# Performance work log

Hardware: AMD Instinct MI355X
Metric: run time of the kernel (lower is better)

## Reference

```python
import jax, jax.numpy as jnp
import numpy as np

NUM_HEADS = 12

def setup_inputs() -> dict:
    key = jax.random.key(0)
    ks = jax.random.split(key, 6)
    B, N, C, P = 16, 785, 768, 48
    return {
        "x": jax.random.normal(ks[0], (B, N, C), jnp.float32),
        "qkv_w": jax.random.normal(ks[1], (3 * C, C), jnp.float32) * 0.02,
        "pos_emb": jax.random.normal(ks[2], (N, N, P), jnp.float32) * 0.02,
        "pos_proj_w": jax.random.normal(ks[3], (NUM_HEADS, P), jnp.float32) * 0.02,
        "proj_w": jax.random.normal(ks[4], (C, C), jnp.float32) * 0.02,
        "proj_b": jnp.zeros((C,), jnp.float32),
    }

def reference(x, qkv_w, pos_emb, pos_proj_w, proj_w, proj_b):
    B, N, C = x.shape
    H = NUM_HEADS
    hd = C // H
    scale = hd ** -0.5
    # qkv projection: [B,N,3C] -> q,k,v each [B,H,N,hd]
    qkv = (x @ qkv_w.T).reshape(B, N, 3, H, hd)
    qkv = jnp.transpose(qkv, (2, 0, 3, 1, 4))
    q, k, v = qkv[0], qkv[1], qkv[2]
    # learned relative-position bias: [H,N,N]
    pos_score = jnp.einsum('nmp,hp->hnm', pos_emb, pos_proj_w)
    # attention scores: scale applied AFTER adding bias (matches original)
    attn = (jnp.einsum('bhnd,bhmd->bhnm', q, k) + pos_score[None]) * scale
    attn = jax.nn.softmax(attn, axis=-1)
    out = jnp.einsum('bhnm,bhmd->bhnd', attn, v)
    out = jnp.transpose(out, (0, 2, 1, 3)).reshape(B, N, C)
    return out @ proj_w.T + proj_b
```

## Files before the change

kernel.cpp:

```cpp
#include <hip/hip_runtime.h>
#include <hip/hip_fp16.h>

#define B_ 16
#define N_ 785
#define NP 800
#define C_ 768
#define H_ 12
#define HD_ 64
#define P_ 48
#define M_ (B_*N_)
#define MP_ (B_*NP)
#define POSW 832
#define VTW  832
#define SLOG2E 0.1803368801111244f

#define OFF_Q   0
#define OFF_K   9646080
#define OFF_VT  19292160
#define OFF_POS 29515776
#define OFF_XF  37353216
#define OFF_AO  OFF_XF
#define OFF_WQ  47085312
#define OFF_WP  48854784

struct __align__(16) Half8 { __half h[8]; };
typedef _Float16 half8_t __attribute__((ext_vector_type(8)));
typedef _Float16 half4_t __attribute__((ext_vector_type(4)));
typedef float f32x4 __attribute__((ext_vector_type(4)));

__device__ __forceinline__ void gl16(const void* g, void* l) {
    __builtin_amdgcn_global_load_lds(
        (const __attribute__((address_space(1))) void*)g,
        (__attribute__((address_space(3))) void*)l, 16, 0, 0);
}

__device__ __forceinline__ int xcd_swz(int o, int nwg) {
    const int q = nwg >> 3, r = nwg & 7;
    const int xcd = o & 7, idx = o >> 3;
    const int base = xcd < r ? xcd * (q + 1) : r * (q + 1) + (xcd - r) * q;
    return base + idx;
}

#define NX4 2411520
#define NQ4 442368
#define NP4 147456
#define NTOT4 (NX4+NQ4+NP4)

__global__ __launch_bounds__(256) void convert_f16(
    const float* __restrict__ x, const float* __restrict__ wq,
    const float* __restrict__ wp, _Float16* __restrict__ xo,
    _Float16* __restrict__ wqo, _Float16* __restrict__ wpo)
{
    int i = blockIdx.x * 256 + threadIdx.x;
    const float4* s; _Float16* d; int o;
    if (i < NX4)            { s = (const float4*)x;  d = xo;  o = i; }
    else if (i < NX4 + NQ4) { s = (const float4*)wq; d = wqo; o = i - NX4; }
    else                    { s = (const float4*)wp; d = wpo; o = i - NX4 - NQ4; }
    float4 v = s[o];
    half4_t h = { (_Float16)v.x, (_Float16)v.y, (_Float16)v.z, (_Float16)v.w };
    *(half4_t*)&d[o * 4] = h;
}

#define QKV_NWG (18 * 100)

__global__ __launch_bounds__(256) void qkv_gemm_mfma(
    const _Float16* __restrict__ A, const _Float16* __restrict__ Bw,
    _Float16* __restrict__ qh, _Float16* __restrict__ kh, _Float16* __restrict__ vth)
{
    __shared__ _Float16 Asl[2][128 * 64];
    __shared__ _Float16 Bsl[2][128 * 64];

    const int t  = threadIdx.x;
    const int w  = t >> 6;
    const int l  = t & 63;
    const int lr = l & 15;
    const int lg = l >> 4;
    const int wm = (w >> 1) * 64;
    const int wn = (w & 1) * 64;

    const int g   = xcd_swz(blockIdx.x, QKV_NWG);
    const int nt  = g % 18;
    const int n0  = nt * 128;
    const int mp0 = (g / 18) * 128;
    const int tsel  = nt / 6;
    const bool isV  = (tsel == 2);
    const int nbase = n0 - tsel * 768;

    const int row0 = t >> 2, row1 = 64 + (t >> 2);
    const int within = (t & 3) * 8;
    const int mpa0 = mp0 + row0, mpa1 = mp0 + row1;
    const int xra0 = (mpa0 / NP) * N_ + min(mpa0 % NP, N_ - 1);
    const int xra1 = (mpa1 / NP) * N_ + min(mpa1 % NP, N_ - 1);
    const _Float16* Ag0 = A  + (size_t)xra0 * 768 + within;
    const _Float16* Ag1 = A  + (size_t)xra1 * 768 + within;
    const _Float16* Bg0 = Bw + (size_t)(n0 + row0) * 768 + within;
    const _Float16* Bg1 = Bw + (size_t)(n0 + row1) * 768 + within;
    const int d0 = t * 8, d1 = (t + 256) * 8, d2 = (t + 512) * 8, d3 = (t + 768) * 8;

    f32x4 acc[4][4];
    #pragma unroll
    for (int i = 0; i < 4; ++i)
        #pragma unroll
        for (int j = 0; j < 4; ++j) acc[i][j] = (f32x4){0.f, 0.f, 0.f, 0.f};

    gl16(Ag0, &Asl[0][d0]); gl16(Ag1, &Asl[0][d1]);
    gl16(Ag0 + 32, &Asl[0][d2]); gl16(Ag1 + 32, &Asl[0][d3]);
    gl16(Bg0, &Bsl[0][d0]); gl16(Bg1, &Bsl[0][d1]);
    gl16(Bg0 + 32, &Bsl[0][d2]); gl16(Bg1 + 32, &Bsl[0][d3]);
    __syncthreads();

    for (int it = 0; it < 12; ++it) {
        const int cur = it & 1;
        if (it < 11) {
            const int kn = (it + 1) * 64;
            gl16(Ag0 + kn, &Asl[cur ^ 1][d0]); gl16(Ag1 + kn, &Asl[cur ^ 1][d1]);
            gl16(Ag0 + kn + 32, &Asl[cur ^ 1][d2]); gl16(Ag1 + kn + 32, &Asl[cur ^ 1][d3]);
            gl16(Bg0 + kn, &Bsl[cur ^ 1][d0]); gl16(Bg1 + kn, &Bsl[cur ^ 1][d1]);
            gl16(Bg0 + kn + 32, &Bsl[cur ^ 1][d2]); gl16(Bg1 + kn + 32, &Bsl[cur ^ 1][d3]);
        }
        #pragma unroll
        for (int kk = 0; kk < 2; ++kk) {
            const int kb = kk * 4096;
            half8_t af[4], bf[4];
            #pragma unroll
            for (int i = 0; i < 4; ++i)
                af[i] = *(const half8_t*)&Asl[cur][kb + (wm + i * 16 + lr) * 32 + lg * 8];
            #pragma unroll
            for (int j = 0; j < 4; ++j)
                bf[j] = *(const half8_t*)&Bsl[cur][kb + (wn + j * 16 + lr) * 32 + lg * 8];
            __builtin_amdgcn_s_setprio(1);
            if (!isV) {
                #pragma unroll
                for (int i = 0; i < 4; ++i)
                    #pragma unroll
                    for (int j = 0; j < 4; ++j)
                        acc[i][j] = __builtin_amdgcn_mfma_f32_16x16x32_f16(bf[j], af[i], acc[i][j], 0, 0, 0);
            } else {
                #pragma unroll
                for (int i = 0; i < 4; ++i)
                    #pragma unroll
                    for (int j = 0; j < 4; ++j)
                        acc[i][j] = __builtin_amdgcn_mfma_f32_16x16x32_f16(af[i], bf[j], acc[i][j], 0, 0, 0);
            }
            __builtin_amdgcn_s_setprio(0);
        }
        __syncthreads();
    }

    if (!isV) {
        _Float16* dstb = (tsel == 0) ? qh : kh;
        const float sc  = (tsel == 0) ? SLOG2E : 1.0f;
        #pragma unroll
        for (int i = 0; i < 4; ++i) {
            const int mp = mp0 + wm + i * 16 + lr;
            const int bb = mp / NP;
            const int nn = mp - bb * NP;
            if (nn >= N_) continue;
            #pragma unroll
            for (int j = 0; j < 4; ++j) {
                const int nq = nbase + wn + j * 16 + lg * 4;
                const int hh = nq >> 6, dd = nq & 63;
                half4_t hv = { (_Float16)(acc[i][j][0] * sc), (_Float16)(acc[i][j][1] * sc),
                               (_Float16)(acc[i][j][2] * sc), (_Float16)(acc[i][j][3] * sc) };
                *(half4_t*)(dstb + ((size_t)(bb * H_ + hh) * N_ + nn) * HD_ + dd) = hv;
            }
        }
    } else {
        #pragma unroll
        for (int i = 0; i < 4; ++i) {
            const int mq  = mp0 + wm + i * 16 + lg * 4;
            const int bb  = mq / NP;
            const int nn0 = mq - bb * NP;
            if (nn0 >= N_) continue;
            const bool full = (nn0 + 3) < N_;
            #pragma unroll
            for (int j = 0; j < 4; ++j) {
                const int n  = nbase + wn + j * 16 + lr;
                const int hh = n >> 6, dd = n & 63;
                _Float16* vb = vth + ((size_t)(bb * H_ + hh) * HD_ + dd) * VTW;
                if (full) {
                    half4_t hv = { (_Float16)acc[i][j][0], (_Float16)acc[i][j][1],
                                   (_Float16)acc[i][j][2], (_Float16)acc[i][j][3] };
                    *(half4_t*)(vb + nn0) = hv;
                } else {
                    #pragma unroll
                    for (int r = 0; r < 4; ++r)
                        if (nn0 + r < N_) vb[nn0 + r] = (_Float16)acc[i][j][r];
                }
            }
        }
    }
}

__global__ __launch_bounds__(256) void pos_kernel(
    const float* __restrict__ pe, const float* __restrict__ pw,
    __half* __restrict__ posh)
{
    __shared__ float W[H_][P_];
    const int t = threadIdx.x;
    for (int i = t; i < H_ * P_; i += 256) W[i / P_][i % P_] = pw[i];
    __syncthreads();
    int nm = blockIdx.x * 256 + t;
    if (nm >= N_ * N_) return;
    float e[48];
    const float4* src = (const float4*)(pe + (size_t)nm * 48);
    #pragma unroll
    for (int i = 0; i < 12; ++i) {
        float4 v = src[i];
        e[4*i] = v.x; e[4*i+1] = v.y; e[4*i+2] = v.z; e[4*i+3] = v.w;
    }
    int n = nm / N_, m = nm - n * N_;
    #pragma unroll
    for (int hh = 0; hh < H_; ++hh) {
        float s = 0.f;
        #pragma unroll
        for (int p = 0; p < 48; ++p) s = fmaf(e[p], W[hh][p], s);
        posh[((size_t)hh * N_ + n) * POSW + m] = __float2half(s * SLOG2E);
    }
}

#define NQT 13
#define ATT_NWG (192 * NQT)

__global__ __launch_bounds__(256) void attn_mfma(
    const _Float16* __restrict__ qh, const _Float16* __restrict__ kh,
    const _Float16* __restrict__ vt, const _Float16* __restrict__ posh,
    _Float16* __restrict__ aoh)
{
    __shared__ _Float16 Kl[2][64][72];
    __shared__ _Float16 Vl[2][64][72];

    const int t  = threadIdx.x;
    const int l  = t & 63;
    const int w  = t >> 6;
    const int lr = l & 15;
    const int lg = l >> 4;

    const int g2   = xcd_swz(blockIdx.x, ATT_NWG);
    const int qt   = g2 % NQT;
    const int rest = g2 / NQT;
    const int b    = rest & 15;
    const int h    = rest >> 4;
    const int bh   = b * H_ + h;
    const int n0   = qt * 64;

    const int qrow = n0 + w * 16 + lr;
    const int qrc  = qrow < N_ ? qrow : N_ - 1;
    const _Float16* qbase = qh + ((size_t)bh * N_ + qrc) * HD_;
    const half8_t qf0 = *(const half8_t*)(qbase + lg * 8);
    const half8_t qf1 = *(const half8_t*)(qbase + 32 + lg * 8);

    f32x4 O0 = {0.f,0.f,0.f,0.f}, O1 = O0, O2 = O0, O3 = O0;
    f32x4 lacc = {0.f,0.f,0.f,0.f};
    float m_run = -1e30f;

    const half8_t vones = { (_Float16)1.f, (_Float16)1.f, (_Float16)1.f, (_Float16)1.f,
                            (_Float16)1.f, (_Float16)1.f, (_Float16)1.f, (_Float16)1.f };

    const int srow = t >> 2;
    const int scol = (t & 3) * 16;
    const int vbase = (scol & 32) + ((scol & 16) >> 2);
    const _Float16* kRow = kh + ((size_t)bh * N_) * HD_ + scol;
    const _Float16* vRow = vt + ((size_t)bh * HD_ + srow) * VTW + scol;
    const _Float16* bFrag = posh + ((size_t)h * N_ + qrc) * POSW + lg * 4;

    half8_t rk0, rk1, rv0, rv1;
    half4_t rbc[4], rbn[4];
    {
        const int gm = srow < N_ ? srow : N_ - 1;
        const half8_t* ks = (const half8_t*)(kRow + (size_t)gm * HD_);
        rk0 = ks[0]; rk1 = ks[1];
        const half8_t* vs = (const half8_t*)vRow;
        rv0 = vs[0]; rv1 = vs[1];
        #pragma unroll
        for (int ms = 0; ms < 4; ++ms)
            rbc[ms] = *(const half4_t*)(bFrag + ms * 16);
    }
    *(half8_t*)&Kl[0][srow][scol]     = rk0;
    *(half8_t*)&Kl[0][srow][scol + 8] = rk1;
    {
        _Float16* vd = &Vl[0][srow][vbase];
        *(half4_t*)(vd +  0) = __builtin_shufflevector(rv0, rv0, 0, 1, 2, 3);
        *(half4_t*)(vd +  8) = __builtin_shufflevector(rv0, rv0, 4, 5, 6, 7);
        *(half4_t*)(vd + 16) = __builtin_shufflevector(rv1, rv1, 0, 1, 2, 3);
        *(half4_t*)(vd + 24) = __builtin_shufflevector(rv1, rv1, 4, 5, 6, 7);
    }

    for (int c = 0; c < 13; ++c) {
        const int cur = c & 1;
        __syncthreads();

        if (c < 12) {
            const int m0n = (c + 1) * 64;
            const int gm  = (m0n + srow) < N_ ? (m0n + srow) : N_ - 1;
            const half8_t* ks = (const half8_t*)(kRow + (size_t)gm * HD_);
            rk0 = ks[0]; rk1 = ks[1];
            const half8_t* vs = (const half8_t*)(vRow + m0n);
            rv0 = vs[0]; rv1 = vs[1];
            #pragma unroll
            for (int ms = 0; ms < 4; ++ms)
                rbn[ms] = *(const half4_t*)(bFrag + m0n + ms * 16);
        }

        f32x4 s[4];
        __builtin_amdgcn_s_setprio(1);
        #pragma unroll
        for (int ms = 0; ms < 4; ++ms) {
            f32x4 acc = { (float)rbc[ms][0], (float)rbc[ms][1],
                          (float)rbc[ms][2], (float)rbc[ms][3] };
            half8_t k0 = *(const half8_t*)&Kl[cur][ms * 16 + lr][lg * 8];
            half8_t k1 = *(const half8_t*)&Kl[cur][ms * 16 + lr][32 + lg * 8];
            acc = __builtin_amdgcn_mfma_f32_16x16x32_f16(k0, qf0, acc, 0, 0, 0);
            acc = __builtin_amdgcn_mfma_f32_16x16x32_f16(k1, qf1, acc, 0, 0, 0);
            s[ms] = acc;
        }
        __builtin_amdgcn_s_setprio(0);

        if (c == 12) {
            #pragma unroll
            for (int ms = 0; ms < 4; ++ms)
                #pragma unroll
                for (int r = 0; r < 4; ++r)
                    if (ms * 16 + lg * 4 + r >= 17) s[ms][r] = -1e30f;
        }

        float x0 = fmaxf(fmaxf(s[0][0], s[0][1]), s[0][2]);
        float x1 = fmaxf(fmaxf(s[0][3], s[1][0]), s[1][1]);
        float x2 = fmaxf(fmaxf(s[1][2], s[1][3]), s[2][0]);
        float x3 = fmaxf(fmaxf(s[2][1], s[2][2]), s[2][3]);
        float x4 = fmaxf(fmaxf(s[3][0], s[3][1]), s[3][2]);
        float mq = fmaxf(fmaxf(fmaxf(x0, x1), x2),
                         fmaxf(fmaxf(x3, x4), s[3][3]));

        if (__any(mq > m_run + 8.f)) {
            float v = fmaxf(mq, __shfl_xor(mq, 16));
            v = fmaxf(v, __shfl_xor(v, 32));
            const float mn    = fmaxf(m_run, v);
            const float alpha = exp2f(m_run - mn);
            m_run = mn;
            const float a0 = __shfl(alpha, lg * 4 + 0);
            const float a1 = __shfl(alpha, lg * 4 + 1);
            const float a2 = __shfl(alpha, lg * 4 + 2);
            const float a3 = __shfl(alpha, lg * 4 + 3);
            O0[0]*=a0; O0[1]*=a1; O0[2]*=a2; O0[3]*=a3;
            O1[0]*=a0; O1[1]*=a1; O1[2]*=a2; O1[3]*=a3;
            O2[0]*=a0; O2[1]*=a1; O2[2]*=a2; O2[3]*=a3;
            O3[0]*=a0; O3[1]*=a1; O3[2]*=a2; O3[3]*=a3;
            lacc[0]*=a0; lacc[1]*=a1; lacc[2]*=a2; lacc[3]*=a3;
        }

        float p[4][4];
        #pragma unroll
        for (int ms = 0; ms < 4; ++ms)
            #pragma unroll
            for (int r = 0; r < 4; ++r)
                p[ms][r] = exp2f(s[ms][r] - m_run);

        half8_t pa0 = { (_Float16)p[0][0], (_Float16)p[0][1], (_Float16)p[0][2], (_Float16)p[0][3],
                        (_Float16)p[1][0], (_Float16)p[1][1], (_Float16)p[1][2], (_Float16)p[1][3] };
        half8_t pa1 = { (_Float16)p[2][0], (_Float16)p[2][1], (_Float16)p[2][2], (_Float16)p[2][3],
                        (_Float16)p[3][0], (_Float16)p[3][1], (_Float16)p[3][2], (_Float16)p[3][3] };

        __builtin_amdgcn_s_setprio(1);
        lacc = __builtin_amdgcn_mfma_f32_16x16x32_f16(pa0, vones, lacc, 0, 0, 0);
        lacc = __builtin_amdgcn_mfma_f32_16x16x32_f16(pa1, vones, lacc, 0, 0, 0);
        #pragma unroll
        for (int ds = 0; ds < 4; ++ds) {
            const _Float16* vr = &Vl[cur][ds * 16 + lr][0];
            half8_t vf0 = *(const half8_t*)&vr[lg * 8];
            half8_t vf1 = *(const half8_t*)&vr[32 + lg * 8];
            f32x4& Od = (ds == 0 ? O0 : ds == 1 ? O1 : ds == 2 ? O2 : O3);
            Od = __builtin_amdgcn_mfma_f32_16x16x32_f16(pa0, vf0, Od, 0, 0, 0);
            Od = __builtin_amdgcn_mfma_f32_16x16x32_f16(pa1, vf1, Od, 0, 0, 0);
        }
        __builtin_amdgcn_s_setprio(0);

        if (c < 12) {
            const int nxt = cur ^ 1;
            *(half8_t*)&Kl[nxt][srow][scol]     = rk0;
            *(half8_t*)&Kl[nxt][srow][scol + 8] = rk1;
            _Float16* vd = &Vl[nxt][srow][vbase];
            *(half4_t*)(vd +  0) = __builtin_shufflevector(rv0, rv0, 0, 1, 2, 3);
            *(half4_t*)(vd +  8) = __builtin_shufflevector(rv0, rv0, 4, 5, 6, 7);
            *(half4_t*)(vd + 16) = __builtin_shufflevector(rv1, rv1, 0, 1, 2, 3);
            *(half4_t*)(vd + 24) = __builtin_shufflevector(rv1, rv1, 4, 5, 6, 7);
            #pragma unroll
            for (int ms = 0; ms < 4; ++ms) rbc[ms] = rbn[ms];
        }
    }

    const int bb = bh / H_;
    #pragma unroll
    for (int r = 0; r < 4; ++r) {
        const int n = n0 + w * 16 + lg * 4 + r;
        if (n >= N_) continue;
        const float inv = 1.f / lacc[r];
        _Float16* dst = aoh + ((size_t)(bb * N_ + n)) * C_ + h * HD_;
        dst[0 * 16 + lr] = (_Float16)(O0[r] * inv);
        dst[1 * 16 + lr] = (_Float16)(O1[r] * inv);
        dst[2 * 16 + lr] = (_Float16)(O2[r] * inv);
        dst[3 * 16 + lr] = (_Float16)(O3[r] * inv);
    }
}

#define PROJ_NWG (6 * 99)

__global__ __launch_bounds__(256) void proj_gemm_mfma(
    const _Float16* __restrict__ A, const _Float16* __restrict__ Bw,
    const float* __restrict__ bias, float* __restrict__ out)
{
    __shared__ _Float16 Asl[2][128 * 64];
    __shared__ _Float16 Bsl[2][128 * 64];

    const int t  = threadIdx.x;
    const int w  = t >> 6;
    const int l  = t & 63;
    const int lr = l & 15;
    const int lg = l >> 4;
    const int wm = (w >> 1) * 64;
    const int wn = (w & 1) * 64;

    const int g  = xcd_swz(blockIdx.x, PROJ_NWG);
    const int n0 = (g % 6) * 128;
    const int m0 = (g / 6) * 128;

    const int row0 = t >> 2, row1 = 64 + (t >> 2);
    const int within = (t & 3) * 8;
    const int ma0 = min(m0 + row0, M_ - 1);
    const int ma1 = min(m0 + row1, M_ - 1);
    const _Float16* Ag0 = A  + (size_t)ma0 * 768 + within;
    const _Float16* Ag1 = A  + (size_t)ma1 * 768 + within;
    const _Float16* Bg0 = Bw + (size_t)(n0 + row0) * 768 + within;
    const _Float16* Bg1 = Bw + (size_t)(n0 + row1) * 768 + within;
    const int d0 = t * 8, d1 = (t + 256) * 8, d2 = (t + 512) * 8, d3 = (t + 768) * 8;

    f32x4 acc[4][4];
    #pragma unroll
    for (int i = 0; i < 4; ++i)
        #pragma unroll
        for (int j = 0; j < 4; ++j) acc[i][j] = (f32x4){0.f, 0.f, 0.f, 0.f};

    gl16(Ag0, &Asl[0][d0]); gl16(Ag1, &Asl[0][d1]);
    gl16(Ag0 + 32, &Asl[0][d2]); gl16(Ag1 + 32, &Asl[0][d3]);
    gl16(Bg0, &Bsl[0][d0]); gl16(Bg1, &Bsl[0][d1]);
    gl16(Bg0 + 32, &Bsl[0][d2]); gl16(Bg1 + 32, &Bsl[0][d3]);
    __syncthreads();

    for (int it = 0; it < 12; ++it) {
        const int cur = it & 1;
        if (it < 11) {
            const int kn = (it + 1) * 64;
            gl16(Ag0 + kn, &Asl[cur ^ 1][d0]); gl16(Ag1 + kn, &Asl[cur ^ 1][d1]);
            gl16(Ag0 + kn + 32, &Asl[cur ^ 1][d2]); gl16(Ag1 + kn + 32, &Asl[cur ^ 1][d3]);
            gl16(Bg0 + kn, &Bsl[cur ^ 1][d0]); gl16(Bg1 + kn, &Bsl[cur ^ 1][d1]);
            gl16(Bg0 + kn + 32, &Bsl[cur ^ 1][d2]); gl16(Bg1 + kn + 32, &Bsl[cur ^ 1][d3]);
        }
        #pragma unroll
        for (int kk = 0; kk < 2; ++kk) {
            const int kb = kk * 4096;
            half8_t af[4], bf[4];
            #pragma unroll
            for (int i = 0; i < 4; ++i)
                af[i] = *(const half8_t*)&Asl[cur][kb + (wm + i * 16 + lr) * 32 + lg * 8];
            #pragma unroll
            for (int j = 0; j < 4; ++j)
                bf[j] = *(const half8_t*)&Bsl[cur][kb + (wn + j * 16 + lr) * 32 + lg * 8];
            __builtin_amdgcn_s_setprio(1);
            #pragma unroll
            for (int i = 0; i < 4; ++i)
                #pragma unroll
                for (int j = 0; j < 4; ++j)
                    acc[i][j] = __builtin_amdgcn_mfma_f32_16x16x32_f16(bf[j], af[i], acc[i][j], 0, 0, 0);
            __builtin_amdgcn_s_setprio(0);
        }
        __syncthreads();
    }

    float4 bj4[4];
    #pragma unroll
    for (int j = 0; j < 4; ++j)
        bj4[j] = *(const float4*)&bias[n0 + wn + j * 16 + lg * 4];
    #pragma unroll
    for (int i = 0; i < 4; ++i) {
        const int m = m0 + wm + i * 16 + lr;
        if (m >= M_) continue;
        #pragma unroll
        for (int j = 0; j < 4; ++j) {
            const int nq = n0 + wn + j * 16 + lg * 4;
            float4 o = { acc[i][j][0] + bj4[j].x, acc[i][j][1] + bj4[j].y,
                         acc[i][j][2] + bj4[j].z, acc[i][j][3] + bj4[j].w };
            *(float4*)&out[(size_t)m * 768 + nq] = o;
        }
    }
}

extern "C" void kernel_launch(void* const* d_in, const int* in_sizes, int n_in,
                              void* d_out, int out_size, void* d_ws, size_t ws_size,
                              hipStream_t stream)
{
    const float* x     = (const float*)d_in[0];
    const float* qkv_w = (const float*)d_in[1];
    const float* pe    = (const float*)d_in[2];
    const float* pw    = (const float*)d_in[3];
    const float* pjw   = (const float*)d_in[4];
    const float* pjb   = (const float*)d_in[5];
    float* out = (float*)d_out;

    _Float16* wsh  = (_Float16*)d_ws;
    _Float16* qh   = wsh + OFF_Q;
    _Float16* kh   = wsh + OFF_K;
    _Float16* vth  = wsh + OFF_VT;
    _Float16* posh = wsh + OFF_POS;
    _Float16* xf   = wsh + OFF_XF;
    _Float16* aoh  = wsh + OFF_AO;
    _Float16* wqf  = wsh + OFF_WQ;
    _Float16* wpf  = wsh + OFF_WP;

    convert_f16<<<dim3(NTOT4 / 256), 256, 0, stream>>>(x, qkv_w, pjw, xf, wqf, wpf);
    qkv_gemm_mfma<<<dim3(QKV_NWG), 256, 0, stream>>>(xf, wqf, qh, kh, vth);
    pos_kernel<<<dim3((N_ * N_ + 255) / 256), 256, 0, stream>>>(pe, pw, (__half*)posh);
    attn_mfma<<<dim3(ATT_NWG), 256, 0, stream>>>(qh, kh, vth, posh, aoh);
    proj_gemm_mfma<<<dim3(PROJ_NWG), 256, 0, stream>>>(aoh, wpf, pjb, out);
}
```

Measured before the change: 257.0 us.

## Fuse fp32-to-fp16 conversion of x into QKV GEMM loads; skip first-tile max subtract

The separate conversion pass over x (about 9.6M floats) is removed. The QKV GEMM now loads fp32 x into registers, converts it to fp16 and writes it to LDS after the MFMA work, so the A operand is prefetched through registers while B still uses direct global-to-LDS loads. This saves a full read and write of x, but x is now read in fp32 by each of the 18 column tiles, which doubles the A-side traffic. Separately, the attention softmax starts with m_run=0 and skips the subtraction until the first rescale, which saves a few ALU ops per tile.

```diff
diff --git a/kernel.cpp b/kernel.cpp
--- a/kernel.cpp
+++ b/kernel.cpp
@@ -18,8 +18,7 @@
 #define OFF_K   9646080
 #define OFF_VT  19292160
 #define OFF_POS 29515776
-#define OFF_XF  37353216
-#define OFF_AO  OFF_XF
+#define OFF_AO  37353216
 #define OFF_WQ  47085312
 #define OFF_WP  48854784
 
@@ -32,6 +31,11 @@
     __builtin_amdgcn_global_load_lds(
         (const __attribute__((address_space(1))) void*)g,
         (__attribute__((address_space(3))) void*)l, 16, 0, 0);
+}
+
+__device__ __forceinline__ half8_t cvt8(float4 u, float4 v) {
+    return (half8_t){ (_Float16)u.x, (_Float16)u.y, (_Float16)u.z, (_Float16)u.w,
+                      (_Float16)v.x, (_Float16)v.y, (_Float16)v.z, (_Float16)v.w };
 }
 
 __device__ __forceinline__ int xcd_swz(int o, int nwg) {
@@ -41,21 +45,18 @@
     return base + idx;
 }
 
-#define NX4 2411520
 #define NQ4 442368
 #define NP4 147456
-#define NTOT4 (NX4+NQ4+NP4)
+#define NW4 (NQ4+NP4)
 
 __global__ __launch_bounds__(256) void convert_f16(
-    const float* __restrict__ x, const float* __restrict__ wq,
-    const float* __restrict__ wp, _Float16* __restrict__ xo,
+    const float* __restrict__ wq, const float* __restrict__ wp,
     _Float16* __restrict__ wqo, _Float16* __restrict__ wpo)
 {
     int i = blockIdx.x * 256 + threadIdx.x;
     const float4* s; _Float16* d; int o;
-    if (i < NX4)            { s = (const float4*)x;  d = xo;  o = i; }
-    else if (i < NX4 + NQ4) { s = (const float4*)wq; d = wqo; o = i - NX4; }
-    else                    { s = (const float4*)wp; d = wpo; o = i - NX4 - NQ4; }
+    if (i < NQ4) { s = (const float4*)wq; d = wqo; o = i; }
+    else         { s = (const float4*)wp; d = wpo; o = i - NQ4; }
     float4 v = s[o];
     half4_t h = { (_Float16)v.x, (_Float16)v.y, (_Float16)v.z, (_Float16)v.w };
     *(half4_t*)&d[o * 4] = h;
@@ -64,7 +65,7 @@
 #define QKV_NWG (18 * 100)
 
 __global__ __launch_bounds__(256) void qkv_gemm_mfma(
-    const _Float16* __restrict__ A, const _Float16* __restrict__ Bw,
+    const float* __restrict__ Ax, const _Float16* __restrict__ Bw,
     _Float16* __restrict__ qh, _Float16* __restrict__ kh, _Float16* __restrict__ vth)
 {
     __shared__ _Float16 Asl[2][128 * 64];
@@ -91,8 +92,8 @@
     const int mpa0 = mp0 + row0, mpa1 = mp0 + row1;
     const int xra0 = (mpa0 / NP) * N_ + min(mpa0 % NP, N_ - 1);
     const int xra1 = (mpa1 / NP) * N_ + min(mpa1 % NP, N_ - 1);
-    const _Float16* Ag0 = A  + (size_t)xra0 * 768 + within;
-    const _Float16* Ag1 = A  + (size_t)xra1 * 768 + within;
+    const float* Ag0 = Ax + (size_t)xra0 * 768 + within;
+    const float* Ag1 = Ax + (size_t)xra1 * 768 + within;
     const _Float16* Bg0 = Bw + (size_t)(n0 + row0) * 768 + within;
     const _Float16* Bg1 = Bw + (size_t)(n0 + row1) * 768 + within;
     const int d0 = t * 8, d1 = (t + 256) * 8, d2 = (t + 512) * 8, d3 = (t + 768) * 8;
@@ -103,18 +104,31 @@
         #pragma unroll
         for (int j = 0; j < 4; ++j) acc[i][j] = (f32x4){0.f, 0.f, 0.f, 0.f};
 
-    gl16(Ag0, &Asl[0][d0]); gl16(Ag1, &Asl[0][d1]);
-    gl16(Ag0 + 32, &Asl[0][d2]); gl16(Ag1 + 32, &Asl[0][d3]);
+    float4 ra[4][2];
+    auto loadA = [&](int kn) {
+        ra[0][0] = *(const float4*)(Ag0 + kn);      ra[0][1] = *(const float4*)(Ag0 + kn + 4);
+        ra[1][0] = *(const float4*)(Ag1 + kn);      ra[1][1] = *(const float4*)(Ag1 + kn + 4);
+        ra[2][0] = *(const float4*)(Ag0 + kn + 32); ra[2][1] = *(const float4*)(Ag0 + kn + 36);
+        ra[3][0] = *(const float4*)(Ag1 + kn + 32); ra[3][1] = *(const float4*)(Ag1 + kn + 36);
+    };
+    auto writeA = [&](int buf) {
+        *(half8_t*)&Asl[buf][d0] = cvt8(ra[0][0], ra[0][1]);
+        *(half8_t*)&Asl[buf][d1] = cvt8(ra[1][0], ra[1][1]);
+        *(half8_t*)&Asl[buf][d2] = cvt8(ra[2][0], ra[2][1]);
+        *(half8_t*)&Asl[buf][d3] = cvt8(ra[3][0], ra[3][1]);
+    };
+
+    loadA(0);
     gl16(Bg0, &Bsl[0][d0]); gl16(Bg1, &Bsl[0][d1]);
     gl16(Bg0 + 32, &Bsl[0][d2]); gl16(Bg1 + 32, &Bsl[0][d3]);
+    writeA(0);
     __syncthreads();
 
     for (int it = 0; it < 12; ++it) {
         const int cur = it & 1;
         if (it < 11) {
             const int kn = (it + 1) * 64;
-            gl16(Ag0 + kn, &Asl[cur ^ 1][d0]); gl16(Ag1 + kn, &Asl[cur ^ 1][d1]);
-            gl16(Ag0 + kn + 32, &Asl[cur ^ 1][d2]); gl16(Ag1 + kn + 32, &Asl[cur ^ 1][d3]);
+            loadA(kn);
             gl16(Bg0 + kn, &Bsl[cur ^ 1][d0]); gl16(Bg1 + kn, &Bsl[cur ^ 1][d1]);
             gl16(Bg0 + kn + 32, &Bsl[cur ^ 1][d2]); gl16(Bg1 + kn + 32, &Bsl[cur ^ 1][d3]);
         }
@@ -144,6 +158,7 @@
             }
             __builtin_amdgcn_s_setprio(0);
         }
+        if (it < 11) writeA(cur ^ 1);
         __syncthreads();
     }
 
@@ -252,7 +267,8 @@
 
     f32x4 O0 = {0.f,0.f,0.f,0.f}, O1 = O0, O2 = O0, O3 = O0;
     f32x4 lacc = {0.f,0.f,0.f,0.f};
-    float m_run = -1e30f;
+    float m_run = 0.f;
+    bool  virgin = true;
 
     const half8_t vones = { (_Float16)1.f, (_Float16)1.f, (_Float16)1.f, (_Float16)1.f,
                             (_Float16)1.f, (_Float16)1.f, (_Float16)1.f, (_Float16)1.f };
@@ -338,6 +354,7 @@
             const float mn    = fmaxf(m_run, v);
             const float alpha = exp2f(m_run - mn);
             m_run = mn;
+            virgin = false;
             const float a0 = __shfl(alpha, lg * 4 + 0);
             const float a1 = __shfl(alpha, lg * 4 + 1);
             const float a2 = __shfl(alpha, lg * 4 + 2);
@@ -350,11 +367,19 @@
         }
 
         float p[4][4];
-        #pragma unroll
-        for (int ms = 0; ms < 4; ++ms)
-            #pragma unroll
-            for (int r = 0; r < 4; ++r)
-                p[ms][r] = exp2f(s[ms][r] - m_run);
+        if (virgin) {
+            #pragma unroll
+            for (int ms = 0; ms < 4; ++ms)
+                #pragma unroll
+                for (int r = 0; r < 4; ++r)
+                    p[ms][r] = exp2f(s[ms][r]);
+        } else {
+            #pragma unroll
+            for (int ms = 0; ms < 4; ++ms)
+                #pragma unroll
+                for (int r = 0; r < 4; ++r)
+                    p[ms][r] = exp2f(s[ms][r] - m_run);
+        }
 
         half8_t pa0 = { (_Float16)p[0][0], (_Float16)p[0][1], (_Float16)p[0][2], (_Float16)p[0][3],
                         (_Float16)p[1][0], (_Float16)p[1][1], (_Float16)p[1][2], (_Float16)p[1][3] };
@@ -511,13 +536,12 @@
     _Float16* kh   = wsh + OFF_K;
     _Float16* vth  = wsh + OFF_VT;
     _Float16* posh = wsh + OFF_POS;
-    _Float16* xf   = wsh + OFF_XF;
     _Float16* aoh  = wsh + OFF_AO;
     _Float16* wqf  = wsh + OFF_WQ;
     _Float16* wpf  = wsh + OFF_WP;
 
-    convert_f16<<<dim3(NTOT4 / 256), 256, 0, stream>>>(x, qkv_w, pjw, xf, wqf, wpf);
-    qkv_gemm_mfma<<<dim3(QKV_NWG), 256, 0, stream>>>(xf, wqf, qh, kh, vth);
+    convert_f16<<<dim3(NW4 / 256), 256, 0, stream>>>(qkv_w, pjw, wqf, wpf);
+    qkv_gemm_mfma<<<dim3(QKV_NWG), 256, 0, stream>>>(x, wqf, qh, kh, vth);
     pos_kernel<<<dim3((N_ * N_ + 255) / 256), 256, 0, stream>>>(pe, pw, (__half*)posh);
     attn_mfma<<<dim3(ATT_NWG), 256, 0, stream>>>(qh, kh, vth, posh, aoh);
     proj_gemm_mfma<<<dim3(PROJ_NWG), 256, 0, stream>>>(aoh, wpf, pjb, out);
```

After: 257.6 us. About the same (+0.2%).
